# Optimization experiments

Hardware: AMD Instinct MI355X
Metric: run time of the kernel (lower is better)

The kernel has to match this reference:

```python
import jax, jax.numpy as jnp
import numpy as np

B, T, F = 2, 128, 88          # batch, time frames, pitch bins (hard-coded 88)
HIDDEN = 64                    # LSTM input dim
N_UNIT = 64                    # channel dim (= 2 * lstm hidden 32)
N_HEAD = 4
HEAD_DIM = N_UNIT // N_HEAD    # 16
WINDOW = 7
N_LAYERS = 2
DIFF_STEPS = 100
LSTM_H = N_UNIT // 2           # 32 per direction


def setup_inputs() -> dict:
    key = jax.random.key(0)
    ks = jax.random.split(key, 12)
    s = 0.05
    inp = {
        'x': jax.random.normal(ks[0], (B, T * F, HIDDEN), jnp.float32),
        't': jax.random.randint(ks[1], (B,), 0, DIFF_STEPS, jnp.int32),
        # LSTM params, stacked [layer, direction, ...]; layer-1 input dim == 2*LSTM_H == HIDDEN
        'lstm_w_ih': s * jax.random.normal(ks[2], (N_LAYERS, 2, 4 * LSTM_H, HIDDEN), jnp.float32),
        'lstm_w_hh': s * jax.random.normal(ks[3], (N_LAYERS, 2, 4 * LSTM_H, LSTM_H), jnp.float32),
        'lstm_b_ih': s * jax.random.normal(ks[4], (N_LAYERS, 2, 4 * LSTM_H), jnp.float32),
        'lstm_b_hh': s * jax.random.normal(ks[5], (N_LAYERS, 2, 4 * LSTM_H), jnp.float32),
        # per-NA-layer params
        't_emb': s * jax.random.normal(ks[6], (N_LAYERS, DIFF_STEPS, N_UNIT), jnp.float32),
        'w_qkv': s * jax.random.normal(ks[7], (N_LAYERS, N_UNIT, 3 * N_UNIT), jnp.float32),
        'b_qkv': jnp.zeros((N_LAYERS, 3 * N_UNIT), jnp.float32),
        'rpb': s * jax.random.normal(ks[8], (N_LAYERS, N_HEAD, 2 * WINDOW - 1, 2 * WINDOW - 1), jnp.float32),
        'w_proj': s * jax.random.normal(ks[9], (N_LAYERS, N_UNIT, N_UNIT), jnp.float32),
        'b_proj': jnp.zeros((N_LAYERS, N_UNIT), jnp.float32),
    }
    return inp


def _lstm_dir(x, w_ih, w_hh, b_ih, b_hh, reverse):
    # x: [N, T, D]; pytorch gate order i, f, g, o
    N = x.shape[0]
    H = w_hh.shape[1]
    xs = jnp.swapaxes(x, 0, 1)
    if reverse:
        xs = xs[::-1]
    b = b_ih + b_hh
    def step(carry, xt):
        h, c = carry
        g = xt @ w_ih.T + h @ w_hh.T + b
        i, f, gg, o = jnp.split(g, 4, axis=-1)
        c = jax.nn.sigmoid(f) * c + jax.nn.sigmoid(i) * jnp.tanh(gg)
        h = jax.nn.sigmoid(o) * jnp.tanh(c)
        return (h, c), h
    h0 = jnp.zeros((N, H), x.dtype)
    _, hs = jax.lax.scan(step, (h0, h0), xs)
    if reverse:
        hs = hs[::-1]
    return jnp.swapaxes(hs, 0, 1)


def _bilstm(x, w_ih, w_hh, b_ih, b_hh):
    for l in range(w_ih.shape[0]):
        fwd = _lstm_dir(x, w_ih[l, 0], w_hh[l, 0], b_ih[l, 0], b_hh[l, 0], False)
        bwd = _lstm_dir(x, w_ih[l, 1], w_hh[l, 1], b_ih[l, 1], b_hh[l, 1], True)
        x = jnp.concatenate([fwd, bwd], axis=-1)
    return x


def _nbh(L, w):
    # NATTEN-style clamped (non-shrinking) neighborhood window per axis
    i = jnp.arange(L)
    start = jnp.clip(i - w // 2, 0, L - w)
    idx = start[:, None] + jnp.arange(w)[None, :]   # [L, w] absolute neighbor idx
    rel = idx - i[:, None] + (w - 1)                # [L, w] rel-pos-bias idx in [0, 2w-2]
    return idx, rel


def _na2d(x, t_idx, emb, wqkv, bqkv, rpb_l, wproj, bproj):
    # x: [B, Th, Tw, C]; diffusion-step conditioning via learned embedding add
    Bx, Th, Tw, C = x.shape
    h = x + emb[t_idx][:, None, None, :]
    qkv = (h @ wqkv + bqkv).reshape(Bx, Th, Tw, 3, N_HEAD, HEAD_DIM)
    q = jnp.moveaxis(qkv[..., 0, :, :], 3, 1) * (HEAD_DIM ** -0.5)  # [B,h,Th,Tw,d]
    k = jnp.moveaxis(qkv[..., 1, :, :], 3, 1)
    v = jnp.moveaxis(qkv[..., 2, :, :], 3, 1)
    ih, rh = _nbh(Th, WINDOW)
    iw, rw = _nbh(Tw, WINDOW)
    # gather windowed neighbors: [B,h,Th,Tw,w,w,d]
    kn = k[:, :, ih[:, None, :, None], iw[None, :, None, :], :]
    vn = v[:, :, ih[:, None, :, None], iw[None, :, None, :], :]
    bias = rpb_l[:, rh[:, None, :, None], rw[None, :, None, :]]     # [h,Th,Tw,w,w]
    logits = jnp.einsum('bhijd,bhijkld->bhijkl', q, kn) + bias[None]
    attn = jax.nn.softmax(logits.reshape(Bx, N_HEAD, Th, Tw, -1), axis=-1).reshape(logits.shape)
    out = jnp.einsum('bhijkl,bhijkld->bhijd', attn, vn)             # [B,h,Th,Tw,d]
    out = jnp.moveaxis(out, 1, 3).reshape(Bx, Th, Tw, C)
    return out @ wproj + bproj


def reference(x, t, lstm_w_ih, lstm_w_hh, lstm_b_ih, lstm_b_hh,
              t_emb, w_qkv, b_qkv, rpb, w_proj, b_proj):
    Bx = x.shape[0]
    Hin = x.shape[-1]
    Tt = x.shape[1] // F
    h = x.reshape(Bx, Tt, F, Hin).transpose(0, 2, 1, 3).reshape(Bx * F, Tt, Hin)
    h = _bilstm(h, lstm_w_ih, lstm_w_hh, lstm_b_ih, lstm_b_hh)      # [B*88, T, n_unit]
    # -> [B, T, 88, n_unit] 2D grid (height=T, width=88)
    h = h.reshape(Bx, F, Tt, N_UNIT).transpose(0, 2, 1, 3)
    for l in range(N_LAYERS):
        h = h + _na2d(h, t, t_emb[l], w_qkv[l], b_qkv[l], rpb[l], w_proj[l], b_proj[l])
    return h
```

## Files before the change

kernel.cpp:

```cpp
#include <hip/hip_runtime.h>
#include <math.h>

#define B_ 2
#define T_ 128
#define F_ 88
#define HID 64
#define NU 64
#define NH 4
#define HD 16
#define LH 32
#define NSEQ (B_*F_)
#define NTOK (B_*T_*F_)
#define NPOS (T_*F_)

__device__ __forceinline__ float fsig(float x) {
    return __builtin_amdgcn_rcpf(1.0f + __expf(-x));
}
__device__ __forceinline__ float ftanh(float x) {
    return 2.0f * __builtin_amdgcn_rcpf(1.0f + __expf(-2.0f*x)) - 1.0f;
}

template<int LAYER>
__global__ void __launch_bounds__(256, 2) gg_kernel(
    const float* __restrict__ xin,
    const float* __restrict__ w_ih,
    const float* __restrict__ b_ih,
    const float* __restrict__ b_hh,
    float* __restrict__ G)
{
    __shared__ __align__(16) float xts[32][68];
    __shared__ __align__(16) float wsh[256][68];
    __shared__ float bsh[256];
    const int s  = blockIdx.x;
    const int t0 = blockIdx.y * 32;
    const int b = s / F_, f = s % F_;
    const int tid = threadIdx.x;

    for (int n = tid; n < 32*64; n += 256) {
        const int tt = n >> 6, k = n & 63;
        xts[tt][k] = (LAYER == 0)
            ? xin[(((size_t)b*T_ + t0+tt)*F_ + f)*HID + k]
            : xin[((size_t)s*T_ + t0+tt)*HID + k];
    }
    for (int n = tid; n < 256*64; n += 256) {
        const int row = n >> 6, k = n & 63;
        wsh[row][k] = w_ih[((size_t)LAYER*256 + row)*HID + k];
    }
    bsh[tid] = b_ih[LAYER*256 + tid] + b_hh[LAYER*256 + tid];
    __syncthreads();

    const int lane = tid & 63;
    const int g    = tid >> 6;
    const int dir  = g >> 1;
    const int th   = g & 1;
    const int rowA = dir*128 + lane;
    const int rowB = dir*128 + 64 + lane;

    float accA[16] = {}, accB[16] = {};
    #pragma unroll 4
    for (int k4 = 0; k4 < 16; k4++) {
        const float4 wA = *(const float4*)&wsh[rowA][k4*4];
        const float4 wB = *(const float4*)&wsh[rowB][k4*4];
        #pragma unroll
        for (int tt = 0; tt < 16; tt++) {
            const float4 xv = *(const float4*)&xts[th*16+tt][k4*4];
            accA[tt] += wA.x*xv.x + wA.y*xv.y + wA.z*xv.z + wA.w*xv.w;
            accB[tt] += wB.x*xv.x + wB.y*xv.y + wB.z*xv.z + wB.w*xv.w;
        }
    }
    const float bA = bsh[rowA], bB = bsh[rowB];
    float2* gout = (float2*)G + ((size_t)(s*2+dir)*T_ + t0 + th*16)*64 + lane;
    #pragma unroll
    for (int tt = 0; tt < 16; tt++) {
        float2 o; o.x = accA[tt] + bA; o.y = accB[tt] + bB;
        gout[(size_t)tt*64] = o;
    }
}

template<int LAYER>
__global__ void __launch_bounds__(128, 1) lstm_rec(
    const float* __restrict__ G,
    const float* __restrict__ w_hh,
    float* __restrict__ outp)
{
    __shared__ float hbuf[T_][NU];
    __shared__ __align__(16) float hstage[2][LH];
    const int s = blockIdx.x;
    const int b = s / F_, f = s % F_;
    const int lane = threadIdx.x & 63;
    const int dir  = threadIdx.x >> 6;

    float2 wh2[LH];
    {
        const float4* pa = (const float4*)(w_hh + ((size_t)(LAYER*2+dir)*128 + lane)*LH);
        const float4* pb = (const float4*)(w_hh + ((size_t)(LAYER*2+dir)*128 + 64 + lane)*LH);
        #pragma unroll
        for (int k4 = 0; k4 < LH/4; k4++) {
            float4 a = pa[k4], c4 = pb[k4];
            wh2[k4*4+0].x=a.x; wh2[k4*4+0].y=c4.x;
            wh2[k4*4+1].x=a.y; wh2[k4*4+1].y=c4.y;
            wh2[k4*4+2].x=a.z; wh2[k4*4+2].y=c4.z;
            wh2[k4*4+3].x=a.w; wh2[k4*4+3].y=c4.w;
        }
    }
    const float2* gp = (const float2*)G + (size_t)(s*2+dir)*T_*64 + lane;
    #define GTIME(st) (dir ? (T_-1-(st)) : (st))

    const float a1 = (lane < LH) ? 2.f : 1.f;
    const float c1 = (lane < LH) ? -1.f : 0.f;

    float h = 0.f, c = 0.f;
    if (lane < LH) hstage[dir][lane] = 0.f;

    #define STEP(gAv, gBv, stepi)                                            \
    {                                                                        \
        float hbc[LH];                                                       \
        _Pragma("unroll")                                                    \
        for (int q = 0; q < LH/4; q++) {                                     \
            const float4 hv = *(const float4*)&hstage[dir][q*4];             \
            hbc[q*4+0]=hv.x; hbc[q*4+1]=hv.y;                                \
            hbc[q*4+2]=hv.z; hbc[q*4+3]=hv.w;                                \
        }                                                                    \
        float aA0 = (gAv), aB0 = (gBv), aA1 = 0.f, aB1 = 0.f;                \
        _Pragma("unroll")                                                    \
        for (int k = 0; k < 16; k++) {                                       \
            aA0 += wh2[k].x*hbc[k];      aB0 += wh2[k].y*hbc[k];             \
            aA1 += wh2[k+16].x*hbc[k+16]; aB1 += wh2[k+16].y*hbc[k+16];      \
        }                                                                    \
        const float accA = aA0 + aA1, accB = aB0 + aB1;                      \
        const float e0 = fsig(accA);                      \
        const float e1 = fmaf(a1, fsig(a1*accB), c1);     \
        const float x0 = __shfl_xor(e0, 32, 64);        \
        const float x1 = __shfl_xor(e1, 32, 64);        \
        c = x0*c + e0*e1;                                                    \
        h = x1 * ftanh(c);                                                   \
        if (lane < LH) {                                                     \
            hbuf[GTIME(stepi)][dir*LH + lane] = h;                           \
            hstage[dir][lane] = h;                                           \
        }                                                                    \
    }

    float2 A[4], Bf[4];
    #pragma unroll
    for (int i = 0; i < 4; i++) A[i]  = gp[(size_t)GTIME(i)*64];
    #pragma unroll
    for (int i = 0; i < 4; i++) Bf[i] = gp[(size_t)GTIME(4+i)*64];

    #pragma unroll 1
    for (int grp = 0; grp < 32; grp++) {
        float2 P[4];
        const int pf = (grp < 30 ? grp + 2 : 31) * 4;
        #pragma unroll
        for (int i = 0; i < 4; i++) P[i] = gp[(size_t)GTIME(pf+i)*64];
        #pragma unroll
        for (int i = 0; i < 4; i++) { STEP(A[i].x, A[i].y, grp*4 + i); }
        #pragma unroll
        for (int i = 0; i < 4; i++) { A[i] = Bf[i]; Bf[i] = P[i]; }
    }
    #undef STEP
    #undef GTIME
    __syncthreads();

    const int tid = threadIdx.x;
    const float4* lds4 = (const float4*)&hbuf[0][0];
    if (LAYER == 0) {
        float4* out4 = (float4*)outp + (size_t)s*T_*16;
        #pragma unroll
        for (int it = 0; it < 16; it++)
            out4[it*128 + tid] = lds4[it*128 + tid];
    } else {
        const int c4 = tid & 15, trow = tid >> 4;
        #pragma unroll
        for (int it = 0; it < 16; it++) {
            const int t = it*8 + trow;
            ((float4*)outp)[(((size_t)b*T_ + t)*F_ + f)*16 + c4] = lds4[t*16 + c4];
        }
    }
}

__global__ void __launch_bounds__(256, 2) qkv_kernel(
    const float* __restrict__ hcur,
    const int*   __restrict__ tarr,
    const float* __restrict__ t_emb,
    const float* __restrict__ w_qkv,
    const float* __restrict__ b_qkv,
    const int layer,
    float* __restrict__ qb, float* __restrict__ kb, float* __restrict__ vb)
{
    __shared__ float as[64][65];
    __shared__ float wsh[64][64];
    const int m0 = blockIdx.x * 64;
    const int which = blockIdx.y;
    const int tid = threadIdx.x;
    const int bidx = m0 / NPOS;
    const int tb = tarr[bidx];
    const float* embp = t_emb + ((size_t)layer*100 + tb)*HID;

    for (int n = tid; n < 64*64; n += 256) {
        const int mm = n >> 6, k = n & 63;
        as[mm][k]  = hcur[((size_t)m0+mm)*64 + k] + embp[k];
        wsh[mm][k] = w_qkv[((size_t)layer*64 + mm)*192 + which*64 + k];
    }
    __syncthreads();

    const int tm = tid >> 4, tn = tid & 15;
    float acc[4][4] = {};
    for (int k = 0; k < 64; k++) {
        const float a0 = as[tm*4+0][k];
        const float a1 = as[tm*4+1][k];
        const float a2 = as[tm*4+2][k];
        const float a3 = as[tm*4+3][k];
        const float4 w = *(const float4*)&wsh[k][tn*4];
        acc[0][0]+=a0*w.x; acc[0][1]+=a0*w.y; acc[0][2]+=a0*w.z; acc[0][3]+=a0*w.w;
        acc[1][0]+=a1*w.x; acc[1][1]+=a1*w.y; acc[1][2]+=a1*w.z; acc[1][3]+=a1*w.w;
        acc[2][0]+=a2*w.x; acc[2][1]+=a2*w.y; acc[2][2]+=a2*w.z; acc[2][3]+=a2*w.w;
        acc[3][0]+=a3*w.x; acc[3][1]+=a3*w.y; acc[3][2]+=a3*w.z; acc[3][3]+=a3*w.w;
    }

    float* dst = (which == 0) ? qb : (which == 1) ? kb : vb;
    const float scale = (which == 0) ? 0.25f : 1.0f;
    const int hh = tn >> 2;
    const int dbase = (tn & 3) * 4;
    const float4 bv = *(const float4*)&b_qkv[(size_t)layer*192 + which*64 + tn*4];
    #pragma unroll
    for (int r = 0; r < 4; r++) {
        const int row = m0 + tm*4 + r;
        const int pos = row - bidx*NPOS;
        float4 o;
        o.x = (acc[r][0] + bv.x) * scale;
        o.y = (acc[r][1] + bv.y) * scale;
        o.z = (acc[r][2] + bv.z) * scale;
        o.w = (acc[r][3] + bv.w) * scale;
        *(float4*)&dst[(((size_t)bidx*NH + hh)*NPOS + pos)*HD + dbase] = o;
    }
}

__global__ void __launch_bounds__(384, 1) nattn_kernel(
    const float* __restrict__ qb,
    const float* __restrict__ kb,
    const float* __restrict__ vb,
    const float* __restrict__ rpb,
    const int layer,
    float* __restrict__ ao)
{
    __shared__ float kv[2][10][88][20];
    __shared__ float rp[169];
    const int blk = blockIdx.x;
    const int bh = blk & 7;
    const int it = blk >> 3;
    const int i0 = it*4;
    const int h  = bh & 3;
    const int bb = bh >> 2;
    const int tid = threadIdx.x;
    const int rs = min(max(i0-3, 0), T_-10);
    const float* kbase = kb + (size_t)bh*NPOS*HD;
    const float* vbase = vb + (size_t)bh*NPOS*HD;

    const bool act = (tid < 4*F_);
    const int isub = act ? (tid / F_) : 0;
    const int j    = act ? (tid - isub*F_) : 0;
    const int i    = i0 + isub;
    const int ihs  = min(max(i-3, 0), T_-7);
    const int ro   = ihs - rs;
    const int cw   = min(max(j-3, 0), F_-7);

    float4 q0, q1, q2, q3;
    if (act) {
        const float4* qp = (const float4*)&qb[((size_t)bh*NPOS + i*F_ + j)*HD];
        q0 = qp[0]; q1 = qp[1]; q2 = qp[2]; q3 = qp[3];
    }
    for (int n = tid; n < 169; n += 384)
        rp[n] = rpb[((size_t)layer*NH + h)*169 + n];
    for (int n4 = tid; n4 < 10*88*4; n4 += 384) {
        const int d4   = n4 & 3;
        const int rest = n4 >> 2;
        const int c    = rest % 88;
        const int r    = rest / 88;
        const size_t goff = ((size_t)(rs+r)*F_ + c)*HD + d4*4;
        *(float4*)&kv[0][r][c][d4*4] = *(const float4*)&kbase[goff];
        *(float4*)&kv[1][r][c][d4*4] = *(const float4*)&vbase[goff];
    }
    __syncthreads();

    if (act) {
        float lg[49];
        #pragma unroll
        for (int ki = 0; ki < 7; ki++) {
            const int rh = ihs + ki - i + 6;
            #pragma unroll
            for (int kj = 0; kj < 7; kj++) {
                const float4* kp = (const float4*)&kv[0][ro+ki][cw+kj][0];
                const float4 k0 = kp[0], k1 = kp[1], k2 = kp[2], k3 = kp[3];
                float d = q0.x*k0.x + q0.y*k0.y + q0.z*k0.z + q0.w*k0.w
                        + q1.x*k1.x + q1.y*k1.y + q1.z*k1.z + q1.w*k1.w
                        + q2.x*k2.x + q2.y*k2.y + q2.z*k2.z + q2.w*k2.w
                        + q3.x*k3.x + q3.y*k3.y + q3.z*k3.z + q3.w*k3.w;
                lg[ki*7+kj] = d + rp[rh*13 + (cw + kj - j + 6)];
            }
        }
        float m = lg[0];
        #pragma unroll
        for (int n = 1; n < 49; n++) m = fmaxf(m, lg[n]);
        float ssum = 0.f;
        #pragma unroll
        for (int n = 0; n < 49; n++) { lg[n] = __expf(lg[n] - m); ssum += lg[n]; }
        const float inv = __builtin_amdgcn_rcpf(ssum);
        #pragma unroll
        for (int n = 0; n < 49; n++) lg[n] *= inv;

        float4 o0 = {0,0,0,0}, o1 = {0,0,0,0}, o2 = {0,0,0,0}, o3 = {0,0,0,0};
        #pragma unroll
        for (int ki = 0; ki < 7; ki++) {
            #pragma unroll
            for (int kj = 0; kj < 7; kj++) {
                const float a = lg[ki*7+kj];
                const float4* vp = (const float4*)&kv[1][ro+ki][cw+kj][0];
                const float4 v0 = vp[0], v1 = vp[1], v2 = vp[2], v3 = vp[3];
                o0.x += a*v0.x; o0.y += a*v0.y; o0.z += a*v0.z; o0.w += a*v0.w;
                o1.x += a*v1.x; o1.y += a*v1.y; o1.z += a*v1.z; o1.w += a*v1.w;
                o2.x += a*v2.x; o2.y += a*v2.y; o2.z += a*v2.z; o2.w += a*v2.w;
                o3.x += a*v3.x; o3.y += a*v3.y; o3.z += a*v3.z; o3.w += a*v3.w;
            }
        }
        float4* op = (float4*)&ao[(((size_t)bb*T_ + i)*F_ + j)*NU + h*HD];
        op[0]=o0; op[1]=o1; op[2]=o2; op[3]=o3;
    }
}

__global__ void __launch_bounds__(256, 2) proj_kernel(
    const float* __restrict__ ain,
    const float* __restrict__ hres,
    const float* __restrict__ w_proj,
    const float* __restrict__ b_proj,
    const int layer,
    float* __restrict__ outp)
{
    __shared__ float as[64][65];
    __shared__ float wsh[64][64];
    const int m0 = blockIdx.x * 64;
    const int tid = threadIdx.x;
    for (int n = tid; n < 64*64; n += 256) {
        const int mm = n >> 6, k = n & 63;
        as[mm][k]  = ain[((size_t)m0+mm)*64 + k];
        wsh[mm][k] = w_proj[(size_t)layer*4096 + n];
    }
    __syncthreads();
    const int tm = tid >> 4, tn = tid & 15;
    float acc[4][4] = {};
    for (int k = 0; k < 64; k++) {
        const float a0 = as[tm*4+0][k];
        const float a1 = as[tm*4+1][k];
        const float a2 = as[tm*4+2][k];
        const float a3 = as[tm*4+3][k];
        const float4 w = *(const float4*)&wsh[k][tn*4];
        acc[0][0]+=a0*w.x; acc[0][1]+=a0*w.y; acc[0][2]+=a0*w.z; acc[0][3]+=a0*w.w;
        acc[1][0]+=a1*w.x; acc[1][1]+=a1*w.y; acc[1][2]+=a1*w.z; acc[1][3]+=a1*w.w;
        acc[2][0]+=a2*w.x; acc[2][1]+=a2*w.y; acc[2][2]+=a2*w.z; acc[2][3]+=a2*w.w;
        acc[3][0]+=a3*w.x; acc[3][1]+=a3*w.y; acc[3][2]+=a3*w.z; acc[3][3]+=a3*w.w;
    }
    const float4 bv = *(const float4*)&b_proj[(size_t)layer*64 + tn*4];
    #pragma unroll
    for (int r = 0; r < 4; r++) {
        const int row = m0 + tm*4 + r;
        const float4 hv = *(const float4*)&hres[(size_t)row*64 + tn*4];
        float4 o;
        o.x = hv.x + acc[r][0] + bv.x;
        o.y = hv.y + acc[r][1] + bv.y;
        o.z = hv.z + acc[r][2] + bv.z;
        o.w = hv.w + acc[r][3] + bv.w;
        *(float4*)&outp[(size_t)row*64 + tn*4] = o;
    }
}

extern "C" void kernel_launch(void* const* d_in, const int* in_sizes, int n_in,
                              void* d_out, int out_size, void* d_ws, size_t ws_size,
                              hipStream_t stream) {
    const float* x      = (const float*)d_in[0];
    const int*   tarr   = (const int*)  d_in[1];
    const float* w_ih   = (const float*)d_in[2];
    const float* w_hh   = (const float*)d_in[3];
    const float* b_ih   = (const float*)d_in[4];
    const float* b_hh   = (const float*)d_in[5];
    const float* t_emb  = (const float*)d_in[6];
    const float* w_qkv  = (const float*)d_in[7];
    const float* b_qkv  = (const float*)d_in[8];
    const float* rpb    = (const float*)d_in[9];
    const float* w_proj = (const float*)d_in[10];
    const float* b_proj = (const float*)d_in[11];

    float* ws   = (float*)d_ws;
    const size_t CH = (size_t)NTOK * NU;
    float* hcur = ws;
    float* h0   = ws + CH;
    float* G    = ws + 2*CH;
    float* qbuf = ws + 2*CH;
    float* kbuf = ws + 3*CH;
    float* vbuf = ws + 4*CH;
    float* ao   = ws + 5*CH;
    float* outp = (float*)d_out;

    gg_kernel<0><<<dim3(NSEQ, T_/32), 256, 0, stream>>>(x,  w_ih, b_ih, b_hh, G);
    lstm_rec<0><<<NSEQ, 128, 0, stream>>>(G, w_hh, h0);
    gg_kernel<1><<<dim3(NSEQ, T_/32), 256, 0, stream>>>(h0, w_ih, b_ih, b_hh, G);
    lstm_rec<1><<<NSEQ, 128, 0, stream>>>(G, w_hh, hcur);

    for (int l = 0; l < 2; l++) {
        qkv_kernel<<<dim3(NTOK/64, 3), 256, 0, stream>>>(
            hcur, tarr, t_emb, w_qkv, b_qkv, l, qbuf, kbuf, vbuf);
        nattn_kernel<<<(T_/4)*8, 384, 0, stream>>>(
            qbuf, kbuf, vbuf, rpb, l, ao);
        proj_kernel<<<NTOK/64, 256, 0, stream>>>(
            ao, hcur, w_proj, b_proj, l, (l == 0) ? hcur : outp);
    }
}
```

Baseline: 241.4 us.

## Store neighborhood-attention K/V tiles in shared memory as bf16 with smaller blocks

The neighborhood attention kernel now converts K and V to bf16 when staging them into shared memory, halving LDS footprint and read traffic. Each block covers 2 query rows with 192 threads instead of 4 rows with 384, and the grid doubles to compensate. This lowers per-block LDS use so two blocks can share a CU, but it adds conversion arithmetic and more redundant halo loading. K and V are rounded to bf16, so attention outputs lose precision.

Measured after the change: 250.8 us. 3.9% more time.

```diff
diff --git a/kernel.cpp b/kernel.cpp
--- a/kernel.cpp
+++ b/kernel.cpp
@@ -19,6 +19,11 @@
 __device__ __forceinline__ float ftanh(float x) {
     return 2.0f * __builtin_amdgcn_rcpf(1.0f + __expf(-2.0f*x)) - 1.0f;
 }
+__device__ __forceinline__ unsigned short bfr(float x) {
+    return (unsigned short)((__float_as_uint(x) + 0x8000u) >> 16);
+}
+__device__ __forceinline__ float blo(unsigned int u) { return __uint_as_float(u << 16); }
+__device__ __forceinline__ float bhi(unsigned int u) { return __uint_as_float(u & 0xffff0000u); }
 
 template<int LAYER>
 __global__ void __launch_bounds__(256, 2) gg_kernel(
@@ -128,10 +133,10 @@
             aA1 += wh2[k+16].x*hbc[k+16]; aB1 += wh2[k+16].y*hbc[k+16];      \
         }                                                                    \
         const float accA = aA0 + aA1, accB = aB0 + aB1;                      \
-        const float e0 = fsig(accA);                      \
-        const float e1 = fmaf(a1, fsig(a1*accB), c1);     \
-        const float x0 = __shfl_xor(e0, 32, 64);        \
-        const float x1 = __shfl_xor(e1, 32, 64);        \
+        const float e0 = fsig(accA);                                         \
+        const float e1 = fmaf(a1, fsig(a1*accB), c1);                        \
+        const float x0 = __shfl_xor(e0, 32, 64);                             \
+        const float x1 = __shfl_xor(e1, 32, 64);                             \
         c = x0*c + e0*e1;                                                    \
         h = x1 * ftanh(c);                                                   \
         if (lane < LH) {                                                     \
@@ -235,7 +240,7 @@
     }
 }
 
-__global__ void __launch_bounds__(384, 1) nattn_kernel(
+__global__ void __launch_bounds__(192, 2) nattn_kernel(
     const float* __restrict__ qb,
     const float* __restrict__ kb,
     const float* __restrict__ vb,
@@ -243,20 +248,20 @@
     const int layer,
     float* __restrict__ ao)
 {
-    __shared__ float kv[2][10][88][20];
+    __shared__ __align__(16) unsigned short kvs[2][8][88][16];
     __shared__ float rp[169];
     const int blk = blockIdx.x;
     const int bh = blk & 7;
     const int it = blk >> 3;
-    const int i0 = it*4;
+    const int i0 = it*2;
     const int h  = bh & 3;
     const int bb = bh >> 2;
     const int tid = threadIdx.x;
-    const int rs = min(max(i0-3, 0), T_-10);
+    const int rs = min(max(i0-3, 0), T_-8);
     const float* kbase = kb + (size_t)bh*NPOS*HD;
     const float* vbase = vb + (size_t)bh*NPOS*HD;
 
-    const bool act = (tid < 4*F_);
+    const bool act = (tid < 2*F_);
     const int isub = act ? (tid / F_) : 0;
     const int j    = act ? (tid - isub*F_) : 0;
     const int i    = i0 + isub;
@@ -269,16 +274,21 @@
         const float4* qp = (const float4*)&qb[((size_t)bh*NPOS + i*F_ + j)*HD];
         q0 = qp[0]; q1 = qp[1]; q2 = qp[2]; q3 = qp[3];
     }
-    for (int n = tid; n < 169; n += 384)
+    for (int n = tid; n < 169; n += 192)
         rp[n] = rpb[((size_t)layer*NH + h)*169 + n];
-    for (int n4 = tid; n4 < 10*88*4; n4 += 384) {
+    for (int n4 = tid; n4 < 8*88*4; n4 += 192) {
         const int d4   = n4 & 3;
         const int rest = n4 >> 2;
         const int c    = rest % 88;
         const int r    = rest / 88;
         const size_t goff = ((size_t)(rs+r)*F_ + c)*HD + d4*4;
-        *(float4*)&kv[0][r][c][d4*4] = *(const float4*)&kbase[goff];
-        *(float4*)&kv[1][r][c][d4*4] = *(const float4*)&vbase[goff];
+        const float4 kf = *(const float4*)&kbase[goff];
+        const float4 vf = *(const float4*)&vbase[goff];
+        ushort4 k4s, v4s;
+        k4s.x = bfr(kf.x); k4s.y = bfr(kf.y); k4s.z = bfr(kf.z); k4s.w = bfr(kf.w);
+        v4s.x = bfr(vf.x); v4s.y = bfr(vf.y); v4s.z = bfr(vf.z); v4s.w = bfr(vf.w);
+        *(ushort4*)&kvs[0][r][c][d4*4] = k4s;
+        *(ushort4*)&kvs[1][r][c][d4*4] = v4s;
     }
     __syncthreads();
 
@@ -289,12 +299,12 @@
             const int rh = ihs + ki - i + 6;
             #pragma unroll
             for (int kj = 0; kj < 7; kj++) {
-                const float4* kp = (const float4*)&kv[0][ro+ki][cw+kj][0];
-                const float4 k0 = kp[0], k1 = kp[1], k2 = kp[2], k3 = kp[3];
-                float d = q0.x*k0.x + q0.y*k0.y + q0.z*k0.z + q0.w*k0.w
-                        + q1.x*k1.x + q1.y*k1.y + q1.z*k1.z + q1.w*k1.w
-                        + q2.x*k2.x + q2.y*k2.y + q2.z*k2.z + q2.w*k2.w
-                        + q3.x*k3.x + q3.y*k3.y + q3.z*k3.z + q3.w*k3.w;
+                const uint4* kp = (const uint4*)&kvs[0][ro+ki][cw+kj][0];
+                const uint4 a = kp[0], b2 = kp[1];
+                float d = q0.x*blo(a.x)  + q0.y*bhi(a.x)  + q0.z*blo(a.y)  + q0.w*bhi(a.y)
+                        + q1.x*blo(a.z)  + q1.y*bhi(a.z)  + q1.z*blo(a.w)  + q1.w*bhi(a.w)
+                        + q2.x*blo(b2.x) + q2.y*bhi(b2.x) + q2.z*blo(b2.y) + q2.w*bhi(b2.y)
+                        + q3.x*blo(b2.z) + q3.y*bhi(b2.z) + q3.z*blo(b2.w) + q3.w*bhi(b2.w);
                 lg[ki*7+kj] = d + rp[rh*13 + (cw + kj - j + 6)];
             }
         }
@@ -308,22 +318,29 @@
         #pragma unroll
         for (int n = 0; n < 49; n++) lg[n] *= inv;
 
-        float4 o0 = {0,0,0,0}, o1 = {0,0,0,0}, o2 = {0,0,0,0}, o3 = {0,0,0,0};
+        float o[16] = {};
         #pragma unroll
         for (int ki = 0; ki < 7; ki++) {
             #pragma unroll
             for (int kj = 0; kj < 7; kj++) {
                 const float a = lg[ki*7+kj];
-                const float4* vp = (const float4*)&kv[1][ro+ki][cw+kj][0];
-                const float4 v0 = vp[0], v1 = vp[1], v2 = vp[2], v3 = vp[3];
-                o0.x += a*v0.x; o0.y += a*v0.y; o0.z += a*v0.z; o0.w += a*v0.w;
-                o1.x += a*v1.x; o1.y += a*v1.y; o1.z += a*v1.z; o1.w += a*v1.w;
-                o2.x += a*v2.x; o2.y += a*v2.y; o2.z += a*v2.z; o2.w += a*v2.w;
-                o3.x += a*v3.x; o3.y += a*v3.y; o3.z += a*v3.z; o3.w += a*v3.w;
+                const uint4* vp = (const uint4*)&kvs[1][ro+ki][cw+kj][0];
+                const uint4 va = vp[0], vb2 = vp[1];
+                o[0]  += a*blo(va.x);  o[1]  += a*bhi(va.x);
+                o[2]  += a*blo(va.y);  o[3]  += a*bhi(va.y);
+                o[4]  += a*blo(va.z);  o[5]  += a*bhi(va.z);
+                o[6]  += a*blo(va.w);  o[7]  += a*bhi(va.w);
+                o[8]  += a*blo(vb2.x); o[9]  += a*bhi(vb2.x);
+                o[10] += a*blo(vb2.y); o[11] += a*bhi(vb2.y);
+                o[12] += a*blo(vb2.z); o[13] += a*bhi(vb2.z);
+                o[14] += a*blo(vb2.w); o[15] += a*bhi(vb2.w);
             }
         }
         float4* op = (float4*)&ao[(((size_t)bb*T_ + i)*F_ + j)*NU + h*HD];
-        op[0]=o0; op[1]=o1; op[2]=o2; op[3]=o3;
+        op[0] = make_float4(o[0],  o[1],  o[2],  o[3]);
+        op[1] = make_float4(o[4],  o[5],  o[6],  o[7]);
+        op[2] = make_float4(o[8],  o[9],  o[10], o[11]);
+        op[3] = make_float4(o[12], o[13], o[14], o[15]);
     }
 }
 
@@ -407,7 +424,7 @@
     for (int l = 0; l < 2; l++) {
         qkv_kernel<<<dim3(NTOK/64, 3), 256, 0, stream>>>(
             hcur, tarr, t_emb, w_qkv, b_qkv, l, qbuf, kbuf, vbuf);
-        nattn_kernel<<<(T_/4)*8, 384, 0, stream>>>(
+        nattn_kernel<<<(T_/2)*8, 192, 0, stream>>>(
             qbuf, kbuf, vbuf, rpb, l, ao);
         proj_kernel<<<NTOK/64, 256, 0, stream>>>(
             ao, hcur, w_proj, b_proj, l, (l == 0) ? hcur : outp);
```
